# Performance work log

Hardware: AMD Instinct MI355X
Metric: run time of the kernel (lower is better)

The kernel has to match this reference:

```python
import jax, jax.numpy as jnp
import numpy as np


def setup_inputs() -> dict:
    key = jax.random.key(0)
    k1, k2 = jax.random.split(key)
    B, N, E, D = 8, 2048, 64, 128
    spatial_embedding = jax.random.normal(k1, (B, N, E), dtype=jnp.float32)
    z = jax.random.normal(k2, (B, N, D), dtype=jnp.float32)
    return {"spatial_embedding": spatial_embedding, "z": z}


def reference(spatial_embedding, z):
    # Pairwise squared L2 distance via ||a||^2 + ||b||^2 - 2 a.b
    # (same math as (e0-e1).norm(2,-1)**2, avoids [B,N,N,E] intermediate)
    sq = jnp.sum(spatial_embedding * spatial_embedding, axis=-1)  # [B,N]
    inner = jnp.einsum('bie,bje->bij', spatial_embedding, spatial_embedding)
    d2 = jnp.maximum(sq[:, :, None] + sq[:, None, :] - 2.0 * inner, 0.0)  # [B,N,N]
    sim = jnp.exp(-d2)
    attn = sim / jnp.sum(sim, axis=-1, keepdims=True)
    out = jnp.einsum('bij,bjd->bid', attn, z)
    return out
```

## Files before the change

kernel.cpp:

```cpp
#include <hip/hip_runtime.h>
#include <hip/hip_bf16.h>

#define BB 8
#define NN 2048
#define EE 64
#define DD 128
#define BN (BB * NN)

typedef __attribute__((ext_vector_type(8))) short short8v;
typedef __attribute__((ext_vector_type(4))) float float4v;

__device__ __forceinline__ short f2bf(float f) {
    __hip_bfloat16 h = __float2bfloat16(f);
    return *reinterpret_cast<short*>(&h);
}
__device__ __forceinline__ uint32_t pack2bf(float a, float b) {
    return (uint32_t)(uint16_t)f2bf(a) | ((uint32_t)(uint16_t)f2bf(b) << 16);
}

#define GLD16(gp, lp)                                                          \
    __builtin_amdgcn_global_load_lds(                                          \
        (const __attribute__((address_space(1))) void*)(gp),                   \
        (__attribute__((address_space(3))) void*)(lp), 16, 0, 0)
#define GLD4(gp, lp)                                                           \
    __builtin_amdgcn_global_load_lds(                                          \
        (const __attribute__((address_space(1))) void*)(gp),                   \
        (__attribute__((address_space(3))) void*)(lp), 4, 0, 0)

__global__ __launch_bounds__(256) void prep_kernel(const float* __restrict__ emb,
                                                   const float* __restrict__ z,
                                                   short* __restrict__ embq,
                                                   short* __restrict__ zq,
                                                   float* __restrict__ sq) {
    __shared__ float zl[64 * 129];
    const int bid = blockIdx.x;
    const int t = threadIdx.x;

    if (bid < 512) {
        int gid = bid * 256 + t;
        int s = gid & 63;
        int ke = (gid >> 6) & 1;
        int r16 = (gid >> 7) & 127;
        int b = gid >> 14;
        int i = r16 * 16 + (s & 15);
        int e0 = ke * 32 + ((s >> 4) & 3) * 8;
        const float4* src = reinterpret_cast<const float4*>(emb + ((size_t)(b * NN + i)) * EE + e0);
        float4 v0 = src[0], v1 = src[1];
        short8v o;
        o[0] = f2bf(v0.x); o[1] = f2bf(v0.y); o[2] = f2bf(v0.z); o[3] = f2bf(v0.w);
        o[4] = f2bf(v1.x); o[5] = f2bf(v1.y); o[6] = f2bf(v1.z); o[7] = f2bf(v1.w);
        *reinterpret_cast<short8v*>(embq + (size_t)gid * 8) = o;
    } else if (bid < 768) {
        int v = bid - 512;
        int b = v >> 5;
        int jt = v & 31;
        int jb = jt * 64;
#pragma unroll
        for (int k = 0; k < 8; ++k) {
            int idx = t + k * 256;
            int jl = idx >> 5, c4 = idx & 31;
            float4 w = reinterpret_cast<const float4*>(z + ((size_t)(b * NN + jb + jl)) * DD)[c4];
            float* p = &zl[jl * 129 + c4 * 4];
            p[0] = w.x; p[1] = w.y; p[2] = w.z; p[3] = w.w;
        }
        __syncthreads();
#pragma unroll
        for (int k = 0; k < 4; ++k) {
            int sid = t + k * 256;
            int blk = sid >> 6, s = sid & 63;
            int ktl = blk >> 3, nt = blk & 7;
            int d = nt * 16 + (s & 15);
            int jl = ktl * 32 + ((s >> 4) & 3) * 8;
            short8v o;
#pragma unroll
            for (int e = 0; e < 8; ++e) o[e] = f2bf(zl[(jl + e) * 129 + d]);
            *reinterpret_cast<short8v*>(zq + ((size_t)((b * 64 + jt * 2 + ktl) * 8 + nt) * 64 + s) * 8) = o;
        }
    } else {
        int v = bid - 768;
        int q = t & 15;
#pragma unroll
        for (int p = 0; p < 4; ++p) {
            int row = v * 64 + p * 16 + (t >> 4);
            float4 rv = reinterpret_cast<const float4*>(emb + (size_t)row * EE)[q];
            float a0 = __bfloat162float(__float2bfloat16(rv.x));
            float a1 = __bfloat162float(__float2bfloat16(rv.y));
            float a2 = __bfloat162float(__float2bfloat16(rv.z));
            float a3 = __bfloat162float(__float2bfloat16(rv.w));
            float s2 = a0 * a0 + a1 * a1 + a2 * a2 + a3 * a3;
#pragma unroll
            for (int off = 1; off < 16; off <<= 1) s2 += __shfl_xor(s2, off);
            if (q == 0) sq[row] = s2;
        }
    }
}

__global__ __launch_bounds__(256, 4) void attn_mfma(const short* __restrict__ embq,
                                                    const short* __restrict__ zq,
                                                    const float* __restrict__ sq,
                                                    float* __restrict__ outnum,
                                                    float* __restrict__ den,
                                                    int njs) {
    __shared__ short sU[4][1024];
    __shared__ int4 sEmbJ[2][512];
    __shared__ float sSqJ[2][64];

    const int t = threadIdx.x;
    const int bid = blockIdx.x;
    const int b = bid & 7;
    const int q = bid >> 3;
    const int it = q & 31;
    const int js = q >> 5;
    const int ib = it * 64;
    const int w = t >> 6;
    const int l = t & 63;
    const int g = (l >> 4) & 3;
    const int c = l & 15;

    const int4* embqI4 = (const int4*)embq;
    const short8v* zq8 = (const short8v*)zq;
    const float* sqB = sq + b * NN;

    const int ntiles = 32 / njs;
    const int jt0 = js * ntiles;
    const int jtEnd = jt0 + ntiles;

    int4* sUi = (int4*)&sU[0][0];

    {
        const int4* srcI = embqI4 + (size_t)(b * 128 + it * 4) * 2 * 64;
        GLD16(srcI + t, sUi + t);
        GLD16(srcI + t + 256, sUi + t + 256);
        const int4* srcJ = embqI4 + (size_t)(b * 128 + jt0 * 4) * 2 * 64;
        GLD16(srcJ + t, &sEmbJ[0][t]);
        GLD16(srcJ + t + 256, &sEmbJ[0][t + 256]);
        if (t < 64) GLD4(sqB + jt0 * 64 + t, &sSqJ[0][t]);
    }
    __syncthreads();

    short8v qkB[2];
    qkB[0] = *reinterpret_cast<const short8v*>(&sUi[(w * 2 + 0) * 64 + l]);
    qkB[1] = *reinterpret_cast<const short8v*>(&sUi[(w * 2 + 1) * 64 + l]);
    const float sqi = sqB[ib + w * 16 + c];

    float dsum = 0.f;
    float4v acc[8];
#pragma unroll
    for (int nt = 0; nt < 8; ++nt) acc[nt] = (float4v){0.f, 0.f, 0.f, 0.f};

    char* ptw = (char*)&sU[w][0];
    const int swz = (c & 7) << 4;

    int cur = 0;
    for (int jt = jt0; jt < jtEnd; ++jt, cur ^= 1) {
        {
            int jn = (jt + 1 < jtEnd) ? jt + 1 : jt;
            int nxt = cur ^ 1;
            const int4* srcJ = embqI4 + (size_t)(b * 128 + jn * 4) * 2 * 64;
            GLD16(srcJ + t, &sEmbJ[nxt][t]);
            GLD16(srcJ + t + 256, &sEmbJ[nxt][t + 256]);
            if (t < 64) GLD4(sqB + jn * 64 + t, &sSqJ[nxt][t]);
        }

        float d2v[4][4];
        float d2minJ[4];
#pragma unroll
        for (int J = 0; J < 4; ++J) {
            short8v a0 = *reinterpret_cast<const short8v*>(&sEmbJ[cur][(J * 2 + 0) * 64 + l]);
            short8v a1 = *reinterpret_cast<const short8v*>(&sEmbJ[cur][(J * 2 + 1) * 64 + l]);
            float4v sfr = (float4v){0.f, 0.f, 0.f, 0.f};
            sfr = __builtin_amdgcn_mfma_f32_16x16x32_bf16(a0, qkB[0], sfr, 0, 0, 0);
            sfr = __builtin_amdgcn_mfma_f32_16x16x32_bf16(a1, qkB[1], sfr, 0, 0, 0);
            float4 sqj = *reinterpret_cast<const float4*>(&sSqJ[cur][J * 16 + 4 * g]);
            d2v[J][0] = fmaxf(fmaf(-2.0f, sfr[0], sqi + sqj.x), 0.0f);
            d2v[J][1] = fmaxf(fmaf(-2.0f, sfr[1], sqi + sqj.y), 0.0f);
            d2v[J][2] = fmaxf(fmaf(-2.0f, sfr[2], sqi + sqj.z), 0.0f);
            d2v[J][3] = fmaxf(fmaf(-2.0f, sfr[3], sqi + sqj.w), 0.0f);
            d2minJ[J] = fminf(fminf(d2v[J][0], d2v[J][1]), fminf(d2v[J][2], d2v[J][3]));
        }
        float tmin = fminf(fminf(d2minJ[0], d2minJ[1]), fminf(d2minJ[2], d2minJ[3]));

        if (!__all(tmin > 13.8f)) {
#pragma unroll
            for (int J = 0; J < 4; ++J) {
                unsigned long long pword = 0ull;
                if (!__all(d2minJ[J] > 13.8f)) {
                    float p0 = __expf(-d2v[J][0]);
                    float p1 = __expf(-d2v[J][1]);
                    float p2 = __expf(-d2v[J][2]);
                    float p3 = __expf(-d2v[J][3]);
                    dsum += (p0 + p1) + (p2 + p3);
                    pword = (unsigned long long)pack2bf(p0, p1) |
                            ((unsigned long long)pack2bf(p2, p3) << 32);
                }
                *reinterpret_cast<unsigned long long*>(
                    ptw + ((c * 128 + g * 8) ^ swz ^ (J * 32))) = pword;
            }
            short8v pa0 = *reinterpret_cast<const short8v*>(ptw + ((c * 128 + 0 * 64 + g * 16) ^ swz));
            short8v pa1 = *reinterpret_cast<const short8v*>(ptw + ((c * 128 + 1 * 64 + g * 16) ^ swz));
#pragma unroll
            for (int nt = 0; nt < 8; ++nt) {
                short8v z0 = zq8[(size_t)((b * 64 + jt * 2 + 0) * 8 + nt) * 64 + l];
                short8v z1 = zq8[(size_t)((b * 64 + jt * 2 + 1) * 8 + nt) * 64 + l];
                acc[nt] = __builtin_amdgcn_mfma_f32_16x16x32_bf16(pa0, z0, acc[nt], 0, 0, 0);
                acc[nt] = __builtin_amdgcn_mfma_f32_16x16x32_bf16(pa1, z1, acc[nt], 0, 0, 0);
            }
        }

        __syncthreads();
    }

    dsum += __shfl_xor(dsum, 16);
    dsum += __shfl_xor(dsum, 32);

    if (njs == 1) {
        float invr[4];
#pragma unroll
        for (int r = 0; r < 4; ++r) invr[r] = 1.0f / __shfl(dsum, 4 * g + r);
#pragma unroll
        for (int r = 0; r < 4; ++r) {
            size_t row = (size_t)(b * NN + ib + w * 16 + 4 * g + r);
#pragma unroll
            for (int nt = 0; nt < 8; ++nt)
                outnum[row * DD + nt * 16 + c] = acc[nt][r] * invr[r];
        }
    } else {
        if (l < 16) den[(size_t)js * BN + b * NN + ib + w * 16 + l] = dsum;
        if (!__all(dsum < 1e-6f)) {
#pragma unroll
            for (int r = 0; r < 4; ++r) {
                size_t row = (size_t)js * BN + b * NN + ib + w * 16 + 4 * g + r;
#pragma unroll
                for (int nt = 0; nt < 8; ++nt)
                    outnum[row * DD + nt * 16 + c] = acc[nt][r];
            }
        }
    }
}

__global__ __launch_bounds__(256) void reduce_kernel(const float4* __restrict__ num,
                                                     const float* __restrict__ den,
                                                     float4* __restrict__ out,
                                                     int njs) {
    int i4 = blockIdx.x * 256 + threadIdx.x;
    int row = i4 >> 5;
    float4 ns = make_float4(0.f, 0.f, 0.f, 0.f);
    float ds = 0.f;
    for (int js = 0; js < njs; ++js) {
        float dj = den[(size_t)js * BN + row];
        ds += dj;
        if (dj >= 1e-6f) {
            float4 v = num[(size_t)js * ((size_t)BN * (DD / 4)) + i4];
            ns.x += v.x; ns.y += v.y; ns.z += v.z; ns.w += v.w;
        }
    }
    float inv = 1.0f / ds;
    out[i4] = make_float4(ns.x * inv, ns.y * inv, ns.z * inv, ns.w * inv);
}

extern "C" void kernel_launch(void* const* d_in, const int* in_sizes, int n_in,
                              void* d_out, int out_size, void* d_ws, size_t ws_size,
                              hipStream_t stream) {
    (void)in_sizes; (void)n_in; (void)out_size;
    const float* emb = (const float*)d_in[0];
    const float* z = (const float*)d_in[1];
    float* out = (float*)d_out;
    float* ws = (float*)d_ws;

    int njs = 1;
    if (ws_size >= 40ull * 1024 * 1024) njs = 4;
    else if (ws_size >= 24ull * 1024 * 1024) njs = 2;

    float* sqw = ws;
    float* denw = ws + BN;
    float* numw = denw + (size_t)njs * BN;
    size_t numFloats = (njs > 1) ? (size_t)njs * BN * DD : 0;
    short* embqw = (short*)(numw + numFloats);
    short* zqw = embqw + (size_t)BB * NN * EE;

    prep_kernel<<<1024, 256, 0, stream>>>(emb, z, embqw, zqw, sqw);

    attn_mfma<<<8 * 32 * njs, 256, 0, stream>>>(embqw, zqw, sqw,
                                                njs == 1 ? out : numw, denw, njs);

    if (njs > 1) {
        reduce_kernel<<<(BN * (DD / 4)) / 256, 256, 0, stream>>>(
            (const float4*)numw, denw, (float4*)out, njs);
    }
}
```

Before: 29.46 us.

## Prefetch J tiles two ahead with explicit vmcnt waits and split barriers

Restructures the J-tile staging so loads run two tiles ahead. Each iteration waits only on the older tile's loads (vmcnt(3)) rather than the full __syncthreads drain, so more memory latency overlaps with compute. Each wave now stages its own copy of the squared norms so every lane issues the same load count, which keeps vmcnt accounting uniform. In exchange there are two barriers per iteration and hand-tuned waitcnt values that depend on how the compiler orders memory operations, which is fragile.

New measurement: 29.61 us. No clear change (+0.5%).

```diff
diff --git a/kernel.cpp b/kernel.cpp
--- a/kernel.cpp
+++ b/kernel.cpp
@@ -103,7 +103,7 @@
                                                     int njs) {
     __shared__ short sU[4][1024];
     __shared__ int4 sEmbJ[2][512];
-    __shared__ float sSqJ[2][64];
+    __shared__ float sSqJ[2][4][64];
 
     const int t = threadIdx.x;
     const int bid = blockIdx.x;
@@ -127,16 +127,24 @@
 
     int4* sUi = (int4*)&sU[0][0];
 
+#define STAGE(buf, tile)                                                       \
+    do {                                                                       \
+        const int4* _sj = embqI4 + (size_t)(b * 128 + (tile) * 4) * 2 * 64;    \
+        GLD16(_sj + t, &sEmbJ[buf][t]);                                        \
+        GLD16(_sj + t + 256, &sEmbJ[buf][t + 256]);                            \
+        GLD4(sqB + (tile) * 64 + l, &sSqJ[buf][w][0]);                         \
+    } while (0)
+
     {
         const int4* srcI = embqI4 + (size_t)(b * 128 + it * 4) * 2 * 64;
         GLD16(srcI + t, sUi + t);
         GLD16(srcI + t + 256, sUi + t + 256);
-        const int4* srcJ = embqI4 + (size_t)(b * 128 + jt0 * 4) * 2 * 64;
-        GLD16(srcJ + t, &sEmbJ[0][t]);
-        GLD16(srcJ + t + 256, &sEmbJ[0][t + 256]);
-        if (t < 64) GLD4(sqB + jt0 * 64 + t, &sSqJ[0][t]);
-    }
-    __syncthreads();
+    }
+    STAGE(0, jt0);
+    STAGE(1, jt0 + 1);
+    asm volatile("s_waitcnt vmcnt(3)" ::: "memory");
+    __builtin_amdgcn_s_barrier();
+    __builtin_amdgcn_sched_barrier(0);
 
     short8v qkB[2];
     qkB[0] = *reinterpret_cast<const short8v*>(&sUi[(w * 2 + 0) * 64 + l]);
@@ -153,15 +161,6 @@
 
     int cur = 0;
     for (int jt = jt0; jt < jtEnd; ++jt, cur ^= 1) {
-        {
-            int jn = (jt + 1 < jtEnd) ? jt + 1 : jt;
-            int nxt = cur ^ 1;
-            const int4* srcJ = embqI4 + (size_t)(b * 128 + jn * 4) * 2 * 64;
-            GLD16(srcJ + t, &sEmbJ[nxt][t]);
-            GLD16(srcJ + t + 256, &sEmbJ[nxt][t + 256]);
-            if (t < 64) GLD4(sqB + jn * 64 + t, &sSqJ[nxt][t]);
-        }
-
         float d2v[4][4];
         float d2minJ[4];
 #pragma unroll
@@ -171,7 +170,7 @@
             float4v sfr = (float4v){0.f, 0.f, 0.f, 0.f};
             sfr = __builtin_amdgcn_mfma_f32_16x16x32_bf16(a0, qkB[0], sfr, 0, 0, 0);
             sfr = __builtin_amdgcn_mfma_f32_16x16x32_bf16(a1, qkB[1], sfr, 0, 0, 0);
-            float4 sqj = *reinterpret_cast<const float4*>(&sSqJ[cur][J * 16 + 4 * g]);
+            float4 sqj = *reinterpret_cast<const float4*>(&sSqJ[cur][w][J * 16 + 4 * g]);
             d2v[J][0] = fmaxf(fmaf(-2.0f, sfr[0], sqi + sqj.x), 0.0f);
             d2v[J][1] = fmaxf(fmaf(-2.0f, sfr[1], sqi + sqj.y), 0.0f);
             d2v[J][2] = fmaxf(fmaf(-2.0f, sfr[2], sqi + sqj.z), 0.0f);
@@ -207,8 +206,17 @@
             }
         }
 
-        __syncthreads();
-    }
+        __builtin_amdgcn_s_barrier();
+        if (jt + 2 < jtEnd) {
+            STAGE(cur, jt + 2);
+            asm volatile("s_waitcnt vmcnt(3)" ::: "memory");
+        } else {
+            asm volatile("s_waitcnt vmcnt(0)" ::: "memory");
+        }
+        __builtin_amdgcn_s_barrier();
+        __builtin_amdgcn_sched_barrier(0);
+    }
+#undef STAGE
 
     dsum += __shfl_xor(dsum, 16);
     dsum += __shfl_xor(dsum, 32);
```
